# Optimization experiments

Hardware: AMD Instinct MI355X
Metric: run time of the kernel (lower is better)

Reference implementation:

```python
import jax, jax.numpy as jnp
import numpy as np
from jax import lax

H = W = 128            # feature map spatial size (2h x 2w)
WIN = 16               # attention window size
DIM = 512
HEADS = 8
DIM_HEAD = 64
INNER = HEADS * DIM_HEAD
SCALE = DIM_HEAD ** -0.5
KEEP = 44
IOU_T = 0.2

_s = np.arange(0, H - WIN + 1, WIN // 2)
_sx, _sy = np.meshgrid(_s, _s)
WINDOWS = np.stack([_sx.ravel(), _sy.ravel(), _sx.ravel() + WIN - 1, _sy.ravel() + WIN - 1], 1).astype(np.float32)
M = WINDOWS.shape[0]   # 225
SX = jnp.asarray(WINDOWS[:, 0].astype(np.int32))
SY = jnp.asarray(WINDOWS[:, 1].astype(np.int32))

# ---- static pairwise IoU (torchvision convention: area=(x2-x1)*(y2-y1)) ----
_x1, _y1, _x2, _y2 = WINDOWS[:, 0], WINDOWS[:, 1], WINDOWS[:, 2], WINDOWS[:, 3]
_area = (_x2 - _x1) * (_y2 - _y1)
_iw = np.clip(np.minimum(_x2[:, None], _x2[None]) - np.maximum(_x1[:, None], _x1[None]), 0, None)
_ih = np.clip(np.minimum(_y2[:, None], _y2[None]) - np.maximum(_y1[:, None], _y1[None]), 0, None)
_inter = _iw * _ih
IOU = jnp.asarray((_inter / (_area[:, None] + _area[None] - _inter)).astype(np.float32))

# ---- roi_align (aligned=False, 1 sample/bin) == separable bilinear resample ----
_bin = (WIN - 1.0) / WIN
_r = (np.arange(WIN) + 0.5) * _bin
_q = np.floor(_r).astype(int)
_f = _r - _q
_A = np.zeros((WIN, WIN), np.float32)
_A[np.arange(WIN), _q] = 1.0 - _f
_A[np.arange(WIN), np.minimum(_q + 1, WIN - 1)] += _f
BILIN = jnp.asarray(_A)


def _nms_select(score):
    """Greedy NMS over the static window set; return first KEEP kept indices."""
    order = jnp.argsort(-score)
    iou_s = IOU[order][:, order]
    def body(i, supp):
        return supp | ((~supp[i]) & (iou_s[i] > IOU_T) & (jnp.arange(M) > i))
    supp = lax.fori_loop(0, M, body, jnp.zeros((M,), dtype=bool))
    pos = jnp.where(~supp, jnp.arange(M), M)
    pos = jnp.minimum(jnp.sort(pos)[:KEEP], M - 1)
    return order[pos]


def setup_inputs() -> dict:
    key = jax.random.key(0)
    k1, k2, k3, k4 = jax.random.split(key, 4)
    x = jax.random.normal(k1, (8, H * W, DIM), dtype=jnp.float32)
    prob = jax.random.uniform(k2, (8, 4, H // 2, W // 2), dtype=jnp.float32)
    W_fix = jnp.ones((1, 1, WIN // 2, WIN // 2), jnp.float32)   # FixCNN ones kernel
    W_qkv = jax.random.normal(k3, (3 * INNER, DIM), jnp.float32) * 0.02
    W_out = jax.random.normal(k4, (DIM, INNER), jnp.float32) * 0.02
    b_out = jnp.zeros((DIM,), jnp.float32)
    return {"x": x, "prob": prob, "W_fix": W_fix, "W_qkv": W_qkv, "W_out": W_out, "b_out": b_out}


def reference(x, prob, W_fix, W_qkv, W_out, b_out):
    b = x.shape[0]
    # entropy over class channels
    entropy = -jnp.sum(prob * jnp.log2(prob + 1e-10), axis=1)           # (b, 64, 64)
    # FixCNN: ones 8x8 kernel, stride 4, then /64
    score = lax.conv(entropy[:, None], W_fix, (WIN // 4, WIN // 4), 'VALID')
    score = (score / float((WIN // 2) ** 2)).reshape(b, -1)             # (b, M)
    x2d = x.transpose(0, 2, 1).reshape(b, DIM, H, W)                    # b d h w
    rng = jnp.arange(WIN)

    def per_batch(feat, sc):
        idx = _nms_select(sc)                                           # (KEEP,)
        sy, sx = SY[idx], SX[idx]
        # gather integer 16x16 patches (box corners are integers)
        patches = jax.vmap(lambda y, xc: lax.dynamic_slice(feat, (0, y, xc), (DIM, WIN, WIN)))(sy, sx)
        # roi_align bilinear resample (separable)
        pat = jnp.einsum('pi,mdij,qj->mdpq', BILIN, patches, BILIN)     # (KEEP, d, 16, 16)
        xi = pat.transpose(0, 2, 3, 1).reshape(KEEP, WIN * WIN, DIM)    # m n d
        qkv = xi @ W_qkv.T
        q, k, v = jnp.split(qkv, 3, axis=-1)
        to_h = lambda t: t.reshape(KEEP, WIN * WIN, HEADS, DIM_HEAD).transpose(0, 2, 1, 3)
        q, k, v = to_h(q), to_h(k), to_h(v)
        attn = jax.nn.softmax(jnp.einsum('mhnd,mhkd->mhnk', q, k) * SCALE, axis=-1)
        out = jnp.einsum('mhnk,mhkd->mhnd', attn, v)
        out = out.transpose(0, 2, 1, 3).reshape(KEEP, WIN * WIN, INNER)
        out = out @ W_out.T + b_out                                     # (KEEP, n, DIM)
        out2d = out.reshape(KEEP, WIN, WIN, DIM).transpose(0, 3, 1, 2)  # m d h w
        yy = sy[:, None, None] + rng[None, :, None]                     # (KEEP,16,1)
        xx = sx[:, None, None] + rng[None, None, :]                     # (KEEP,1,16)
        acc = jnp.zeros((DIM, H, W), x.dtype).at[:, yy, xx].add(out2d.transpose(1, 0, 2, 3))
        cnt = jnp.zeros((H, W), x.dtype).at[yy, xx].add(1.0)
        return acc, cnt

    acc, cnt = jax.vmap(per_batch)(x2d, score)
    outx = (acc / (cnt[:, None] + 1e-10)).reshape(b, DIM, H * W).transpose(0, 2, 1)
    return x + outx
```

## Files before the change

### kernel.cpp

```cpp
#include <hip/hip_runtime.h>
#include <type_traits>
#include <utility>

typedef unsigned short u16;
typedef __attribute__((ext_vector_type(8))) short short8;
typedef __attribute__((ext_vector_type(8))) __bf16 bf16v8;
typedef __attribute__((ext_vector_type(4))) float f32x4;
typedef __attribute__((ext_vector_type(16))) float f32x16;

template <typename T, typename = void> struct mfma_ok : std::false_type {};
template <typename T>
struct mfma_ok<T, std::void_t<decltype(__builtin_amdgcn_mfma_f32_16x16x32_bf16(
    std::declval<T>(), std::declval<T>(), std::declval<f32x4>(), 0, 0, 0))>>
    : std::true_type {};
using frag8 = std::conditional_t<mfma_ok<bf16v8>::value, bf16v8, short8>;

#define MFMA16(a, b, c) __builtin_amdgcn_mfma_f32_16x16x32_bf16((a), (b), (c), 0, 0, 0)
#define MFMA32(a, b, c) __builtin_amdgcn_mfma_f32_32x32x16_bf16((a), (b), (c), 0, 0, 0)

__device__ __forceinline__ float bf2f(u16 u) {
  unsigned v = ((unsigned)u) << 16;
  return __builtin_bit_cast(float, v);
}
__device__ __forceinline__ u16 f2bf(float f) {
  unsigned u = __builtin_bit_cast(unsigned, f);
  u = (u + 0x7fffu + ((u >> 16) & 1u)) >> 16;
  return (u16)u;
}
__device__ __forceinline__ unsigned cvtpk_bf16(float lo, float hi) {
  unsigned r;
  asm("v_cvt_pk_bf16_f32 %0, %1, %2" : "=v"(r) : "v"(lo), "v"(hi));
  return r;
}
__device__ __forceinline__ void gl16(const u16* g, u16* l) {
  __builtin_amdgcn_global_load_lds((__attribute__((address_space(1))) void*)(g),
                                   (__attribute__((address_space(3))) void*)(l), 16, 0, 0);
}

__global__ void k_score(const float* __restrict__ prob, const float* __restrict__ wfix,
                        float* __restrict__ scores) {
  const int b = blockIdx.x, tid = threadIdx.x;
  __shared__ float ent[64 * 64];
  __shared__ float wf[64];
  if (tid < 64) wf[tid] = wfix[tid];
  const float* pb = prob + (size_t)b * 4 * 4096;
  for (int p = tid; p < 4096; p += 256) {
    float e = 0.f;
#pragma unroll
    for (int ch = 0; ch < 4; ++ch) {
      float v = pb[ch * 4096 + p];
      e -= v * log2f(v + 1e-10f);
    }
    ent[p] = e;
  }
  __syncthreads();
  if (tid < 225) {
    int wy = tid / 15, wx = tid % 15;
    float s = 0.f;
    for (int a = 0; a < 8; ++a)
      for (int c = 0; c < 8; ++c)
        s += ent[(wy * 4 + a) * 64 + wx * 4 + c] * wf[a * 8 + c];
    scores[b * 225 + tid] = s * (1.0f / 64.0f);
  }
}

__device__ __forceinline__ float iou_pair(int wa, int wb) {
  float x1a = (float)((wa % 15) * 8), y1a = (float)((wa / 15) * 8);
  float x1b = (float)((wb % 15) * 8), y1b = (float)((wb / 15) * 8);
  float iw = fminf(x1a, x1b) + 15.f - fmaxf(x1a, x1b);
  float ih = fminf(y1a, y1b) + 15.f - fmaxf(y1a, y1b);
  iw = fmaxf(iw, 0.f);
  ih = fmaxf(ih, 0.f);
  float inter = iw * ih;
  return inter / (450.f - inter);
}

__global__ void k_nms(const float* __restrict__ scores, int* __restrict__ sel,
                      int* __restrict__ kept, float* __restrict__ mult) {
  const int b = blockIdx.x, t = threadIdx.x;
  __shared__ float s[225];
  __shared__ int order[225];
  __shared__ unsigned char supp[225];
  __shared__ int idx44[44];
  __shared__ int ks[225];
  __shared__ float ml[225];
  if (t < 225) s[t] = scores[b * 225 + t];
  __syncthreads();
  if (t < 225) {
    float st = s[t];
    int r = 0;
    for (int j = 0; j < 225; ++j) {
      float sj = s[j];
      r += (sj > st) || (sj == st && j < t);
    }
    order[r] = t;
    supp[t] = 0;
    ks[t] = -1;
    ml[t] = 0.f;
  }
  __syncthreads();
  for (int i = 0; i < 224; ++i) {
    if (t > i && t < 225 && !supp[i]) {
      if (iou_pair(order[i], order[t]) > 0.2f) supp[t] = 1;
    }
    __syncthreads();
  }
  if (t == 0) {
    int k = 0;
    for (int i = 0; i < 225 && k < 44; ++i)
      if (!supp[i]) idx44[k++] = order[i];
    while (k < 44) idx44[k++] = order[224];
    for (int k2 = 0; k2 < 44; ++k2) {
      int w = idx44[k2];
      if (ks[w] < 0) ks[w] = k2;
      ml[w] += 1.f;
    }
  }
  __syncthreads();
  if (t < 225) {
    kept[b * 225 + t] = ks[t];
    mult[b * 225 + t] = ml[t];
  }
  if (t < 44) sel[b * 44 + t] = idx44[t];
}

__global__ void k_castw(const float* __restrict__ Wq, const float* __restrict__ Wo,
                        u16* __restrict__ wqb, u16* __restrict__ wob) {
  int idx = blockIdx.x * 256 + threadIdx.x;
  if (idx < 786432) wqb[idx] = f2bf(Wq[idx]);
  int i2 = idx - 786432;
  if (i2 >= 0 && i2 < 262144) wob[i2] = f2bf(Wo[i2]);
}

__global__ __launch_bounds__(256) void k_gather(const float* __restrict__ x,
                                                const int* __restrict__ sel,
                                                u16* __restrict__ xi) {
  const size_t idx = (size_t)blockIdx.x * 256 + threadIdx.x;
  const int dc = (int)(idx & 63);
  const int pq = (int)((idx >> 6) & 255);
  const int g = (int)(idx >> 14);
  const int b = g / 44;
  const int w = sel[g];
  const int sy = (w / 15) * 8, sx = (w % 15) * 8;
  const int p = pq >> 4, q = pq & 15;
  float rp = ((float)p + 0.5f) * 0.9375f;
  int i0 = (int)rp;
  float fp = rp - (float)i0;
  float rq = ((float)q + 0.5f) * 0.9375f;
  int j0 = (int)rq;
  float fq = rq - (float)j0;
  const float w00 = (1.f - fp) * (1.f - fq), w01 = (1.f - fp) * fq;
  const float w10 = fp * (1.f - fq), w11 = fp * fq;
  const float* xb = x + ((size_t)b * 16384 + (size_t)(sy + i0) * 128 + sx + j0) * 512 + dc * 8;
  const float4* t00 = (const float4*)xb;
  const float4* t01 = (const float4*)(xb + 512);
  const float4* t10 = (const float4*)(xb + 512 * 128);
  const float4* t11 = (const float4*)(xb + 512 * 129);
  float acc[8];
#pragma unroll
  for (int h = 0; h < 2; ++h) {
    float4 a = t00[h], bb = t01[h], c = t10[h], d = t11[h];
    acc[h * 4 + 0] = w00 * a.x + w01 * bb.x + w10 * c.x + w11 * d.x;
    acc[h * 4 + 1] = w00 * a.y + w01 * bb.y + w10 * c.y + w11 * d.y;
    acc[h * 4 + 2] = w00 * a.z + w01 * bb.z + w10 * c.z + w11 * d.z;
    acc[h * 4 + 3] = w00 * a.w + w01 * bb.w + w10 * c.w + w11 * d.w;
  }
  short8 o;
#pragma unroll
  for (int e = 0; e < 8; ++e) o[e] = (short)f2bf(acc[e]);
  *(short8*)&xi[((size_t)g * 256 + pq) * 512 + dc * 8] = o;
}

template <int BIAS>
__global__ __launch_bounds__(256) void k_gemm(const u16* __restrict__ A, const u16* __restrict__ B,
                                              u16* __restrict__ C, const float* __restrict__ bias,
                                              int M, int N, int K) {
  __shared__ u16 sA[128 * 32];
  __shared__ u16 sB[128 * 32];
  const int tid = threadIdx.x, lane = tid & 63, wv = tid >> 6;
  const int bn = blockIdx.x, bm = blockIdx.y;
  const int wm = (wv >> 1) * 64, wn = (wv & 1) * 64;
  const int lb0 = wv * 2048, lb1 = wv * 2048 + 1024;
  const int gb0 = lb0 + lane * 16, gb1 = lb1 + lane * 16;
  const int r0 = gb0 >> 6, c0 = (gb0 & 63) >> 1;
  const int r1 = gb1 >> 6, c1 = (gb1 & 63) >> 1;
  const u16* Ag0 = A + (size_t)(bm * 128 + r0) * K + c0;
  const u16* Ag1 = A + (size_t)(bm * 128 + r1) * K + c1;
  const u16* Bg0 = B + (size_t)(bn * 128 + r0) * K + c0;
  const u16* Bg1 = B + (size_t)(bn * 128 + r1) * K + c1;
  u16* lA0 = &sA[lb0 >> 1];
  u16* lA1 = &sA[lb1 >> 1];
  u16* lB0 = &sB[lb0 >> 1];
  u16* lB1 = &sB[lb1 >> 1];
  f32x4 acc[4][4] = {};
  const int ra = wm + (lane & 15), rb = wn + (lane & 15), k8 = (lane >> 4) * 8;
  for (int kt = 0; kt < K; kt += 32) {
    gl16(Ag0 + kt, lA0);
    gl16(Ag1 + kt, lA1);
    gl16(Bg0 + kt, lB0);
    gl16(Bg1 + kt, lB1);
    __syncthreads();
    frag8 af[4], bf[4];
#pragma unroll
    for (int i = 0; i < 4; ++i) af[i] = *(const frag8*)&sA[(ra + i * 16) * 32 + k8];
#pragma unroll
    for (int i = 0; i < 4; ++i) bf[i] = *(const frag8*)&sB[(rb + i * 16) * 32 + k8];
#pragma unroll
    for (int i = 0; i < 4; ++i)
#pragma unroll
      for (int j = 0; j < 4; ++j) acc[i][j] = MFMA16(af[i], bf[j], acc[i][j]);
    __syncthreads();
  }
  const int cc = lane & 15, rr = (lane >> 4) * 4;
#pragma unroll
  for (int i = 0; i < 4; ++i)
#pragma unroll
    for (int j = 0; j < 4; ++j)
#pragma unroll
      for (int e = 0; e < 4; ++e) {
        int row = bm * 128 + wm + i * 16 + rr + e;
        int col = bn * 128 + wn + j * 16 + cc;
        float v = acc[i][j][e];
        if (BIAS) v += bias[col];
        C[(size_t)row * N + col] = f2bf(v);
      }
}

__global__ __launch_bounds__(256, 2) void k_attn(const u16* __restrict__ qkv,
                                                 u16* __restrict__ aout) {
  const int g = blockIdx.x;
  const int win = g >> 3, h = g & 7;
  const int tid = threadIdx.x, lane = tid & 63, wv = tid >> 6;
  const int l31 = lane & 31, l5 = lane >> 5;
  const bool lo32 = (lane < 32);
  __shared__ u16 smem[25344];
  u16* KbB = smem;
  u16* VtB = smem + 8704;
  const u16* base = qkv + (size_t)win * 256 * 1536;
  const u16* kbase = base + 512 + h * 64;
  const u16* vbase = base + 1024 + h * 64;
  const int prow = tid >> 2, pc16 = (tid & 3) * 16;

  {
    const u16* kp = kbase + (size_t)prow * 1536 + pc16;
    *(short8*)&KbB[prow * 68 + pc16] = *(const short8*)kp;
    *(short8*)&KbB[prow * 68 + pc16 + 8] = *(const short8*)(kp + 8);
  }
  {
    const u16* vp = vbase + (size_t)tid * 1536;
#pragma unroll
    for (int c8 = 0; c8 < 64; c8 += 8) {
      short8 v = *(const short8*)(vp + c8);
#pragma unroll
      for (int e2 = 0; e2 < 8; ++e2) VtB[(c8 + e2) * 260 + tid] = (u16)v[e2];
    }
  }
  frag8 qf[2][4];
#pragma unroll
  for (int qt = 0; qt < 2; ++qt)
#pragma unroll
    for (int c = 0; c < 4; ++c)
      qf[qt][c] = *(const frag8*)(base + (size_t)(wv * 64 + qt * 32 + l31) * 1536 + h * 64 +
                                  c * 16 + l5 * 8);
  __syncthreads();

  f32x16 of[2][2] = {};
  float m_run[2] = {-3e38f, -3e38f};
  float l_run[2] = {0.f, 0.f};

  int cur = 0;
  for (int kb = 0; kb < 4; ++kb) {
    short8 pf0 = {}, pf1 = {};
    if (kb < 3) {
      const u16* kp = kbase + (size_t)((kb + 1) * 64 + prow) * 1536 + pc16;
      pf0 = *(const short8*)kp;
      pf1 = *(const short8*)(kp + 8);
    }
#pragma unroll
    for (int qt = 0; qt < 2; ++qt) {
      f32x16 s0 = {}, s1 = {};
#pragma unroll
      for (int c = 0; c < 4; ++c) {
        frag8 kf0 = *(const frag8*)&KbB[cur * 4352 + l31 * 68 + c * 16 + l5 * 8];
        frag8 kf1 = *(const frag8*)&KbB[cur * 4352 + (32 + l31) * 68 + c * 16 + l5 * 8];
        s0 = MFMA32(kf0, qf[qt][c], s0);
        s1 = MFMA32(kf1, qf[qt][c], s1);
      }
      float tm[16];
#pragma unroll
      for (int r = 0; r < 16; ++r) tm[r] = fmaxf(s0[r], s1[r]);
#pragma unroll
      for (int r = 0; r < 8; ++r) tm[r] = fmaxf(tm[r], tm[r + 8]);
#pragma unroll
      for (int r = 0; r < 4; ++r) tm[r] = fmaxf(tm[r], tm[r + 4]);
      float pm = fmaxf(fmaxf(tm[0], tm[1]), fmaxf(tm[2], tm[3]));
      pm = fmaxf(pm, __shfl_xor(pm, 32));
      if (!__all(pm <= m_run[qt] + 64.f)) {
        float mn = fmaxf(m_run[qt], pm);
        float corr = __expf((m_run[qt] - mn) * 0.125f);
        l_run[qt] *= corr;
#pragma unroll
        for (int dt = 0; dt < 2; ++dt)
#pragma unroll
          for (int r = 0; r < 16; ++r) of[qt][dt][r] *= corr;
        m_run[qt] = mn;
      }
      const float mqt = m_run[qt];
      float ls = 0.f;
#pragma unroll
      for (int kt = 0; kt < 2; ++kt) {
        const f32x16 sv = kt ? s1 : s0;
        float p[16];
#pragma unroll
        for (int r = 0; r < 16; ++r) p[r] = __expf((sv[r] - mqt) * 0.125f);
        float e0 = (p[0] + p[1]) + (p[2] + p[3]);
        float e1 = (p[4] + p[5]) + (p[6] + p[7]);
        float e2 = (p[8] + p[9]) + (p[10] + p[11]);
        float e3 = (p[12] + p[13]) + (p[14] + p[15]);
        ls += (e0 + e1) + (e2 + e3);
#pragma unroll
        for (int cc = 0; cc < 2; ++cc) {
          const int bx = cc * 8;
          unsigned a0 = cvtpk_bf16(p[bx + 0], p[bx + 1]);
          unsigned a1 = cvtpk_bf16(p[bx + 2], p[bx + 3]);
          unsigned b0 = cvtpk_bf16(p[bx + 4], p[bx + 5]);
          unsigned b1 = cvtpk_bf16(p[bx + 6], p[bx + 7]);
          unsigned sa0 = __shfl_xor(a0, 32);
          unsigned sa1 = __shfl_xor(a1, 32);
          unsigned sb0 = __shfl_xor(b0, 32);
          unsigned sb1 = __shfl_xor(b1, 32);
          uint4 fu;
          fu.x = lo32 ? a0 : sb0;
          fu.y = lo32 ? a1 : sb1;
          fu.z = lo32 ? sa0 : b0;
          fu.w = lo32 ? sa1 : b1;
          frag8 pb = __builtin_bit_cast(frag8, fu);
#pragma unroll
          for (int dt = 0; dt < 2; ++dt) {
            frag8 va = *(const frag8*)&VtB[(dt * 32 + l31) * 260 + kb * 64 + kt * 32 + cc * 16 +
                                           l5 * 8];
            of[qt][dt] = MFMA32(va, pb, of[qt][dt]);
          }
        }
      }
      l_run[qt] += ls;
    }
    if (kb < 3) {
      *(short8*)&KbB[(cur ^ 1) * 4352 + prow * 68 + pc16] = pf0;
      *(short8*)&KbB[(cur ^ 1) * 4352 + prow * 68 + pc16 + 8] = pf1;
    }
    __syncthreads();
    cur ^= 1;
  }

  float inv[2];
#pragma unroll
  for (int qt = 0; qt < 2; ++qt) {
    float lt = l_run[qt] + __shfl_xor(l_run[qt], 32);
    inv[qt] = 1.0f / lt;
  }
  u16* sc = smem + wv * 4352;
#pragma unroll
  for (int qt = 0; qt < 2; ++qt)
#pragma unroll
    for (int dt = 0; dt < 2; ++dt)
#pragma unroll
      for (int j = 0; j < 4; ++j) {
        unsigned w0 = cvtpk_bf16(of[qt][dt][4 * j + 0] * inv[qt], of[qt][dt][4 * j + 1] * inv[qt]);
        unsigned w1 = cvtpk_bf16(of[qt][dt][4 * j + 2] * inv[qt], of[qt][dt][4 * j + 3] * inv[qt]);
        *(uint2*)&sc[(qt * 32 + l31) * 68 + dt * 32 + 8 * j + 4 * l5] = make_uint2(w0, w1);
      }
  __syncthreads();
#pragma unroll
  for (int rep = 0; rep < 8; ++rep) {
    int row = rep * 8 + (lane >> 3);
    uint2 lo = *(const uint2*)&sc[row * 68 + (lane & 7) * 8];
    uint2 hi = *(const uint2*)&sc[row * 68 + (lane & 7) * 8 + 4];
    *(int4*)&aout[(size_t)(win * 256 + wv * 64 + row) * 512 + h * 64 + (lane & 7) * 8] =
        make_int4((int)lo.x, (int)lo.y, (int)hi.x, (int)hi.y);
  }
}

__global__ void k_final(const float* __restrict__ x, const u16* __restrict__ proj,
                        const int* __restrict__ kept, const float* __restrict__ mult,
                        float* __restrict__ out) {
  const size_t idx = (size_t)blockIdx.x * 256 + threadIdx.x;
  const int dci = (int)(idx & 31);
  const int pix = (int)((idx >> 5) & 16383);
  const int b = (int)(idx >> 19);
  const int y = pix >> 7, xc = pix & 127;
  float acc[16];
#pragma unroll
  for (int e = 0; e < 16; ++e) acc[e] = 0.f;
  float c = 0.f;
  const int wyh = y >> 3, wxh = xc >> 3;
#pragma unroll
  for (int a = 0; a < 2; ++a) {
    int wy = wyh - 1 + a;
    if (wy < 0 || wy > 14) continue;
#pragma unroll
    for (int bb = 0; bb < 2; ++bb) {
      int wx = wxh - 1 + bb;
      if (wx < 0 || wx > 14) continue;
      int w = wy * 15 + wx;
      int slot = kept[b * 225 + w];
      if (slot < 0) continue;
      float ml = mult[b * 225 + w];
      c += ml;
      const u16* pr = proj +
                      ((size_t)((b * 44 + slot) * 256 + (y - wy * 8) * 16 + (xc - wx * 8))) * 512 +
                      (size_t)dci * 16;
      short8 v0 = *(const short8*)pr;
      short8 v1 = *(const short8*)(pr + 8);
#pragma unroll
      for (int e = 0; e < 8; ++e) acc[e] += ml * bf2f((u16)v0[e]);
#pragma unroll
      for (int e = 0; e < 8; ++e) acc[8 + e] += ml * bf2f((u16)v1[e]);
    }
  }
  const float inv = 1.f / (c + 1e-10f);
  const size_t off = ((size_t)(b * 16384 + pix)) * 512 + (size_t)dci * 16;
  const float4* xp = (const float4*)(x + off);
  float4* op = (float4*)(out + off);
#pragma unroll
  for (int q4 = 0; q4 < 4; ++q4) {
    float4 xv = xp[q4];
    float4 ov;
    ov.x = xv.x + acc[q4 * 4 + 0] * inv;
    ov.y = xv.y + acc[q4 * 4 + 1] * inv;
    ov.z = xv.z + acc[q4 * 4 + 2] * inv;
    ov.w = xv.w + acc[q4 * 4 + 3] * inv;
    op[q4] = ov;
  }
}

extern "C" void kernel_launch(void* const* d_in, const int* in_sizes, int n_in, void* d_out,
                              int out_size, void* d_ws, size_t ws_size, hipStream_t stream) {
  const float* x = (const float*)d_in[0];
  const float* prob = (const float*)d_in[1];
  const float* wfix = (const float*)d_in[2];
  const float* Wq = (const float*)d_in[3];
  const float* Wo = (const float*)d_in[4];
  const float* bo = (const float*)d_in[5];
  float* out = (float*)d_out;
  char* ws = (char*)d_ws;

  float* scores = (float*)(ws + 0);
  int* sel = (int*)(ws + 8192);
  int* kept = (int*)(ws + 16384);
  float* mult = (float*)(ws + 24576);
  u16* wqb = (u16*)(ws + 32768);
  u16* wob = (u16*)(ws + 32768 + 1572864);
  u16* xi = (u16*)(ws + 4194304);
  u16* qkv = (u16*)(ws + 4194304 + 92274688);
  u16* aout = xi;
  u16* proj = qkv;

  k_score<<<8, 256, 0, stream>>>(prob, wfix, scores);
  k_nms<<<8, 256, 0, stream>>>(scores, sel, kept, mult);
  k_castw<<<4096, 256, 0, stream>>>(Wq, Wo, wqb, wob);
  k_gather<<<22528, 256, 0, stream>>>(x, sel, xi);
  k_gemm<0><<<dim3(12, 704), 256, 0, stream>>>(xi, wqb, qkv, nullptr, 90112, 1536, 512);
  k_attn<<<2816, 256, 0, stream>>>(qkv, aout);
  k_gemm<1><<<dim3(4, 704), 256, 0, stream>>>(aout, wob, proj, bo, 90112, 512, 512);
  k_final<<<16384, 256, 0, stream>>>(x, proj, kept, mult, out);
}
```

Baseline: 766.5 us.

## Replace GEMM with 256x256 double-buffered tiles and XCD-aware block swizzle

Rewrites both projection GEMMs as a 512-thread kernel computing 256x256 output tiles with BK=64. Global-to-LDS loads are double-buffered with explicit vmcnt waits, so the next K-slice loads while MFMAs run on the current one. Block indices are remapped across the 8 XCDs, and bias is hoisted per column. In exchange it uses 128KB of LDS and more registers per thread, hardcodes K=512 (8 iterations), and lowers the block count (704 for the output projection).

```diff
diff --git a/kernel.cpp b/kernel.cpp
--- a/kernel.cpp
+++ b/kernel.cpp
@@ -36,6 +36,9 @@
   __builtin_amdgcn_global_load_lds((__attribute__((address_space(1))) void*)(g),
                                    (__attribute__((address_space(3))) void*)(l), 16, 0, 0);
 }
+__device__ __forceinline__ void vmw8() { asm volatile("s_waitcnt vmcnt(8)" ::: "memory"); }
+__device__ __forceinline__ void vmw0() { asm volatile("s_waitcnt vmcnt(0)" ::: "memory"); }
+__device__ __forceinline__ void lgw0() { asm volatile("s_waitcnt lgkmcnt(0)" ::: "memory"); }
 
 __global__ void k_score(const float* __restrict__ prob, const float* __restrict__ wfix,
                         float* __restrict__ scores) {
@@ -172,58 +175,92 @@
 }
 
 template <int BIAS>
-__global__ __launch_bounds__(256) void k_gemm(const u16* __restrict__ A, const u16* __restrict__ B,
-                                              u16* __restrict__ C, const float* __restrict__ bias,
-                                              int M, int N, int K) {
-  __shared__ u16 sA[128 * 32];
-  __shared__ u16 sB[128 * 32];
+__global__ __launch_bounds__(512, 2) void k_gemm256(const u16* __restrict__ A,
+                                                    const u16* __restrict__ B, u16* __restrict__ C,
+                                                    const float* __restrict__ bias, int M, int N,
+                                                    int K, int nbn) {
+  __shared__ u16 sA[2][256 * 64];
+  __shared__ u16 sB[2][256 * 64];
   const int tid = threadIdx.x, lane = tid & 63, wv = tid >> 6;
-  const int bn = blockIdx.x, bm = blockIdx.y;
-  const int wm = (wv >> 1) * 64, wn = (wv & 1) * 64;
-  const int lb0 = wv * 2048, lb1 = wv * 2048 + 1024;
-  const int gb0 = lb0 + lane * 16, gb1 = lb1 + lane * 16;
-  const int r0 = gb0 >> 6, c0 = (gb0 & 63) >> 1;
-  const int r1 = gb1 >> 6, c1 = (gb1 & 63) >> 1;
-  const u16* Ag0 = A + (size_t)(bm * 128 + r0) * K + c0;
-  const u16* Ag1 = A + (size_t)(bm * 128 + r1) * K + c1;
-  const u16* Bg0 = B + (size_t)(bn * 128 + r0) * K + c0;
-  const u16* Bg1 = B + (size_t)(bn * 128 + r1) * K + c1;
-  u16* lA0 = &sA[lb0 >> 1];
-  u16* lA1 = &sA[lb1 >> 1];
-  u16* lB0 = &sB[lb0 >> 1];
-  u16* lB1 = &sB[lb1 >> 1];
-  f32x4 acc[4][4] = {};
-  const int ra = wm + (lane & 15), rb = wn + (lane & 15), k8 = (lane >> 4) * 8;
-  for (int kt = 0; kt < K; kt += 32) {
-    gl16(Ag0 + kt, lA0);
-    gl16(Ag1 + kt, lA1);
-    gl16(Bg0 + kt, lB0);
-    gl16(Bg1 + kt, lB1);
-    __syncthreads();
-    frag8 af[4], bf[4];
-#pragma unroll
-    for (int i = 0; i < 4; ++i) af[i] = *(const frag8*)&sA[(ra + i * 16) * 32 + k8];
-#pragma unroll
-    for (int i = 0; i < 4; ++i) bf[i] = *(const frag8*)&sB[(rb + i * 16) * 32 + k8];
-#pragma unroll
-    for (int i = 0; i < 4; ++i)
-#pragma unroll
-      for (int j = 0; j < 4; ++j) acc[i][j] = MFMA16(af[i], bf[j], acc[i][j]);
-    __syncthreads();
-  }
+  const int f = blockIdx.x;
+  const int q8 = gridDim.x >> 3;
+  const int wg = (f & 7) * q8 + (f >> 3);
+  const int bm = wg / nbn, bn = wg % nbn;
+  const int wm = (wv >> 2) * 128, wn = (wv & 3) * 64;
+  const int l15 = lane & 15, k8 = (lane >> 4) * 8;
+  const int srow = tid >> 3, sc8 = (tid & 7) * 8;
+  const u16* Ab = A + (size_t)(bm * 256 + srow) * K + sc8;
+  const u16* Bb = B + (size_t)(bn * 256 + srow) * K + sc8;
+
+  f32x4 acc[8][4] = {};
+
+#define STAGE(kt, buf)                                                       \
+  {                                                                          \
+    const int ko = (kt) * 64;                                                \
+    _Pragma("unroll") for (int c = 0; c < 4; ++c) {                          \
+      gl16(Ab + (size_t)(c * 64) * K + ko, &sA[buf][c * 4096 + wv * 512]);   \
+      gl16(Bb + (size_t)(c * 64) * K + ko, &sB[buf][c * 4096 + wv * 512]);   \
+    }                                                                        \
+  }
+
+  STAGE(0, 0);
+  STAGE(1, 1);
+
+  for (int t = 0; t < 8; ++t) {
+    const int buf = t & 1;
+    if (t == 7)
+      vmw0();
+    else
+      vmw8();
+    __builtin_amdgcn_sched_barrier(0);
+    __builtin_amdgcn_s_barrier();
+#pragma unroll
+    for (int mh = 0; mh < 2; ++mh)
+#pragma unroll
+      for (int nh = 0; nh < 2; ++nh) {
+        frag8 af[4][2], bf[2][2];
+#pragma unroll
+        for (int i = 0; i < 4; ++i)
+#pragma unroll
+          for (int kk = 0; kk < 2; ++kk)
+            af[i][kk] =
+                *(const frag8*)&sA[buf][(wm + (mh * 4 + i) * 16 + l15) * 64 + kk * 32 + k8];
+#pragma unroll
+        for (int j = 0; j < 2; ++j)
+#pragma unroll
+          for (int kk = 0; kk < 2; ++kk)
+            bf[j][kk] =
+                *(const frag8*)&sB[buf][(wn + (nh * 2 + j) * 16 + l15) * 64 + kk * 32 + k8];
+        __builtin_amdgcn_s_setprio(1);
+#pragma unroll
+        for (int i = 0; i < 4; ++i)
+#pragma unroll
+          for (int j = 0; j < 2; ++j)
+#pragma unroll
+            for (int kk = 0; kk < 2; ++kk)
+              acc[mh * 4 + i][nh * 2 + j] = MFMA16(af[i][kk], bf[j][kk], acc[mh * 4 + i][nh * 2 + j]);
+        __builtin_amdgcn_s_setprio(0);
+      }
+    lgw0();
+    __builtin_amdgcn_sched_barrier(0);
+    __builtin_amdgcn_s_barrier();
+    if (t < 6) STAGE(t + 2, buf);
+  }
+#undef STAGE
+
   const int cc = lane & 15, rr = (lane >> 4) * 4;
 #pragma unroll
-  for (int i = 0; i < 4; ++i)
-#pragma unroll
-    for (int j = 0; j < 4; ++j)
+  for (int i = 0; i < 8; ++i)
+#pragma unroll
+    for (int j = 0; j < 4; ++j) {
+      int col = bn * 256 + wn + j * 16 + cc;
+      float badd = BIAS ? bias[col] : 0.f;
 #pragma unroll
       for (int e = 0; e < 4; ++e) {
-        int row = bm * 128 + wm + i * 16 + rr + e;
-        int col = bn * 128 + wn + j * 16 + cc;
-        float v = acc[i][j][e];
-        if (BIAS) v += bias[col];
-        C[(size_t)row * N + col] = f2bf(v);
+        int row = bm * 256 + wm + i * 16 + rr + e;
+        C[(size_t)row * N + col] = f2bf(acc[i][j][e] + badd);
       }
+    }
 }
 
 __global__ __launch_bounds__(256, 2) void k_attn(const u16* __restrict__ qkv,
@@ -460,8 +497,8 @@
   k_nms<<<8, 256, 0, stream>>>(scores, sel, kept, mult);
   k_castw<<<4096, 256, 0, stream>>>(Wq, Wo, wqb, wob);
   k_gather<<<22528, 256, 0, stream>>>(x, sel, xi);
-  k_gemm<0><<<dim3(12, 704), 256, 0, stream>>>(xi, wqb, qkv, nullptr, 90112, 1536, 512);
+  k_gemm256<0><<<2112, 512, 0, stream>>>(xi, wqb, qkv, nullptr, 90112, 1536, 512, 6);
   k_attn<<<2816, 256, 0, stream>>>(qkv, aout);
-  k_gemm<1><<<dim3(4, 704), 256, 0, stream>>>(aout, wob, proj, bo, 90112, 512, 512);
+  k_gemm256<1><<<704, 512, 0, stream>>>(aout, wob, proj, bo, 90112, 512, 512, 2);
   k_final<<<16384, 256, 0, stream>>>(x, proj, kept, mult, out);
 }
```

After: 850.6 us. 1.11x slower.
